# Kernel optimization log

Measured on AMD Instinct MI355X. Metric: run time of the kernel, lower is better.

## Reference

```python
import jax, jax.numpy as jnp
import numpy as np

B, C, P, E, M, H, K = 1024, 8192, 3, 64, 128, 16, 8
SCALE = 0.05
EPS = 1e-12  # tf.math.l2_normalize epsilon


def setup_inputs() -> dict:
    key = jax.random.key(0)
    ks = jax.random.split(key, 16)
    return {
        'pools': jax.random.uniform(ks[0], (B, C), dtype=jnp.float32),            # dense stand-in for SparseTensor batch_pools
        'metapaths': jax.random.uniform(ks[1], (P, C, C), dtype=jnp.float32),     # card-card metapath matrices
        'card_embeddings': jax.random.normal(ks[2], (C, E), dtype=jnp.float32) * SCALE,
        'mp_kernels': jax.random.normal(ks[3], (P, E, M), dtype=jnp.float32) * SCALE,
        'mp_biases': jnp.zeros((P, M, 1), dtype=jnp.float32),
        'Wq': jax.random.normal(ks[4], (M, H, K), dtype=jnp.float32) * SCALE,
        'bq': jnp.zeros((H, K), dtype=jnp.float32),
        'Wk': jax.random.normal(ks[5], (M, H, K), dtype=jnp.float32) * SCALE,
        'bk': jnp.zeros((H, K), dtype=jnp.float32),
        'Wv': jax.random.normal(ks[6], (M, H, K), dtype=jnp.float32) * SCALE,
        'bv': jnp.zeros((H, K), dtype=jnp.float32),
        'Wo': jax.random.normal(ks[7], (H, K, M), dtype=jnp.float32) * SCALE,
        'bo': jnp.zeros((M,), dtype=jnp.float32),
        'pool_kernel': jax.random.normal(ks[8], (M, E), dtype=jnp.float32) * SCALE,
        'pool_bias': jnp.zeros((E,), dtype=jnp.float32),
    }


def _l2_normalize(x, axis):
    # matches tf.math.l2_normalize: x / sqrt(max(sum(x^2), eps))
    sq = jnp.sum(jnp.square(x), axis=axis, keepdims=True)
    return x * jax.lax.rsqrt(jnp.maximum(sq, EPS))


def reference(pools, metapaths, card_embeddings, mp_kernels, mp_biases,
              Wq, bq, Wk, bk, Wv, bv, Wo, bo, pool_kernel, pool_bias):
    # --- MetapathEmbed layers, vectorized over the P metapaths ---
    # path_card_embeddings: act(einsum('ce,em->mc') + bias) -> (P, M, C)
    path_card = jax.nn.silu(jnp.einsum('ce,pem->pmc', card_embeddings, mp_kernels) + mp_biases)
    # path_card_matrix: einsum('mc,cd->dm') -> (P, C, M)
    pcm = jnp.einsum('pmc,pcd->pdm', path_card, metapaths)
    # sparse_dense_matmul(batch_pools, path_card_matrix); stack over metapaths -> (B, P, M)
    x = jnp.einsum('bd,pdm->bpm', pools, pcm)

    # --- keras MultiHeadAttention(query=x, value=x) ---
    q = jnp.einsum('bpm,mhk->bphk', x, Wq) + bq
    k = jnp.einsum('bpm,mhk->bphk', x, Wk) + bk
    v = jnp.einsum('bpm,mhk->bphk', x, Wv) + bv
    scores = jnp.einsum('bphk,bqhk->bhpq', q, k) / np.float32(np.sqrt(K))
    attn = jax.nn.softmax(scores, axis=-1)
    o = jnp.einsum('bhpq,bqhk->bphk', attn, v)
    attended = jnp.einsum('bphk,hkm->bpm', o, Wo) + bo  # (B, P, M)

    # --- pooling head ---
    pre_pool = jnp.sum(attended, axis=1)                       # (B, M)
    pool_embeds = jnp.einsum('bm,me->be', pre_pool, pool_kernel) + pool_bias
    norm_pool = _l2_normalize(pool_embeds, axis=1)             # (B, E)
    norm_cards = _l2_normalize(card_embeddings, axis=1)        # (C, E)
    return (jnp.einsum('be,ce->bc', norm_pool, norm_cards) + 1.0) / 2.0
```

## Files before the change

kernel.cpp:

```cpp
#include <hip/hip_runtime.h>
#include <hip/hip_bf16.h>

typedef unsigned int uint;
typedef unsigned short ushort;
typedef float f32x4 __attribute__((ext_vector_type(4)));
typedef short s16x8 __attribute__((ext_vector_type(8)));
typedef int i32x4 __attribute__((ext_vector_type(4)));
typedef uint u32x2 __attribute__((ext_vector_type(2)));

#define C_DIM 8192
#define B_DIM 1024
#define P_DIM 3
#define E_DIM 64
#define M_DIM 128

#define PCA_OFF   0ull
#define PART_OFF  15728640ull
#define PCMH_OFF  66060288ull
#define PCML_OFF  72351744ull
#define XPART_OFF PART_OFF
#define NPOOL_OFF 78643200ull
#define NCARD_OFF 78774272ull

__device__ __forceinline__ uint bf16_rne(float f) {
  uint u = __builtin_bit_cast(uint, f);
  return (u + 0x7fffu + ((u >> 16) & 1u)) >> 16;
}
__device__ __forceinline__ float bf16_to_f32(uint b) {
  return __builtin_bit_cast(float, b << 16);
}
__device__ __forceinline__ uint pk2(float a, float b) {
  float2 t; t.x = a; t.y = b;
  __hip_bfloat162 h2 = __float22bfloat162_rn(t);
  uint r;
  __builtin_memcpy(&r, &h2, 4);
  return r;
}

__global__ __launch_bounds__(256) void k1_pathcard(
    const float* __restrict__ cardemb, const float* __restrict__ mpk,
    const float* __restrict__ mpbias, ushort* __restrict__ pcA) {
  __shared__ float ce_l[64 * 68];
  const int tid = threadIdx.x;
  const int cb = blockIdx.x;
  const int p  = blockIdx.y;
  for (int r = 0; r < 16; ++r) {
    int i = r * 256 + tid;
    int row = i >> 6, col = i & 63;
    ce_l[row * 68 + col] = cardemb[(size_t)(cb * 64 + row) * 64 + col];
  }
  __syncthreads();
  const int m = tid & 127;
  const int chalf = tid >> 7;
  float kr[64];
#pragma unroll
  for (int e = 0; e < 64; ++e) kr[e] = mpk[(size_t)p * E_DIM * M_DIM + e * M_DIM + m];
  const float bias = mpbias[p * M_DIM + m];
  for (int cl0 = 0; cl0 < 32; ++cl0) {
    int cl = chalf * 32 + cl0;
    float acc = bias;
#pragma unroll
    for (int e = 0; e < 64; ++e) acc += ce_l[cl * 68 + e] * kr[e];
    float s = acc / (1.0f + expf(-acc));
    uint hb = bf16_rne(s);
    uint lb = bf16_rne(s - bf16_to_f32(hb));
    int c = cb * 64 + cl;
    int kt = c >> 5, kl = c & 31;
    size_t off = ((size_t)(p * 256 + kt) * 20480 + (size_t)m * 80 + (size_t)kl * 2) >> 1;
    pcA[off] = (ushort)hb;
    pcA[off + 5120] = (ushort)lb;
  }
}

__global__ __launch_bounds__(256, 3) void k2_big(
    const float* __restrict__ mp, const ushort* __restrict__ pcA,
    float* __restrict__ partial) {
  __shared__ char smem[32768];
  const int tid = threadIdx.x;
  int lin = blockIdx.x + 64 * (blockIdx.y + 4 * blockIdx.z);
  int swz = (lin & 7) * 96 + (lin >> 3);
  const int dt = swz & 63, q = (swz >> 6) & 3, p = swz >> 8;
  const int lane = tid & 63, wid = tid >> 6;
  const int wr = wid >> 1, wc = wid & 1;
  const int r16 = lane & 15, g4 = lane >> 4;
  const float* mpb = mp + (size_t)p * C_DIM * C_DIM + (size_t)dt * 128;
  const char* pcb = (const char*)pcA + (size_t)(p * 256 + q * 64) * 20480;
  const int sd = tid & 127, skh = tid >> 7;
  const int fc = ((sd ^ (sd >> 2)) & 3) << 4;
  const int fr = ((r16 ^ (r16 >> 2)) & 3) << 4;

  f32x4 acc[4][4];
#pragma unroll
  for (int i = 0; i < 4; ++i)
#pragma unroll
    for (int j = 0; j < 4; ++j) acc[i][j] = (f32x4){0.f, 0.f, 0.f, 0.f};

  float br[16];
  s16x8 ahA[4], alA[4], ahB[4], alB[4];

#define LOADA(T, AH, AL)                                                      \
  {                                                                           \
    const char* At_ = pcb + (size_t)(T) * 20480;                              \
    _Pragma("unroll") for (int i = 0; i < 4; ++i) {                           \
      int offa_ = (wr * 64 + i * 16 + r16) * 80 + g4 * 16;                    \
      AH[i] = *(const s16x8*)(At_ + offa_);                                   \
      AL[i] = *(const s16x8*)(At_ + 10240 + offa_);                           \
    }                                                                         \
  }
#define LOADB(T)                                                              \
  {                                                                           \
    int c0_ = q * 2048 + (T) * 32;                                            \
    _Pragma("unroll") for (int ii = 0; ii < 2; ++ii) {                        \
      const float* rp_ = mpb + (size_t)(c0_ + ii * 16 + skh * 8) * C_DIM + sd;\
      _Pragma("unroll") for (int j = 0; j < 8; ++j)                           \
          br[ii * 8 + j] = rp_[(size_t)j * C_DIM];                            \
    }                                                                         \
  }
#define WRITEB(BUF)                                                           \
  {                                                                           \
    char* bb_ = smem + (BUF) * 16384;                                         \
    _Pragma("unroll") for (int ii = 0; ii < 2; ++ii) {                        \
      uint hw_[4], lw_[4];                                                    \
      _Pragma("unroll") for (int k2 = 0; k2 < 4; ++k2) {                      \
        float v0_ = br[ii * 8 + k2 * 2], v1_ = br[ii * 8 + k2 * 2 + 1];       \
        uint h_ = pk2(v0_, v1_);                                              \
        float h0_ = __builtin_bit_cast(float, h_ << 16);                      \
        float h1_ = __builtin_bit_cast(float, h_ & 0xffff0000u);              \
        hw_[k2] = h_;                                                         \
        lw_[k2] = pk2(v0_ - h0_, v1_ - h1_);                                  \
      }                                                                       \
      int off_ = sd * 64 + ((((ii * 2 + skh) << 4)) ^ fc);                    \
      *(i32x4*)(bb_ + off_) =                                                 \
          (i32x4){(int)hw_[0], (int)hw_[1], (int)hw_[2], (int)hw_[3]};        \
      *(i32x4*)(bb_ + 8192 + off_) =                                          \
          (i32x4){(int)lw_[0], (int)lw_[1], (int)lw_[2], (int)lw_[3]};        \
    }                                                                         \
  }
#define MFMAB(BUF, AH, AL)                                                    \
  {                                                                           \
    const char* Bb_ = smem + (BUF) * 16384;                                   \
    _Pragma("unroll") for (int j = 0; j < 4; ++j) {                           \
      int offb_ = (wc * 64 + j * 16 + r16) * 64 + ((g4 << 4) ^ fr);           \
      s16x8 bh_ = *(const s16x8*)(Bb_ + offb_);                               \
      s16x8 bl_ = *(const s16x8*)(Bb_ + 8192 + offb_);                        \
      _Pragma("unroll") for (int i = 0; i < 4; ++i) {                         \
        acc[i][j] =                                                           \
            __builtin_amdgcn_mfma_f32_16x16x32_bf16(AH[i], bh_, acc[i][j], 0, 0, 0); \
        acc[i][j] =                                                           \
            __builtin_amdgcn_mfma_f32_16x16x32_bf16(AH[i], bl_, acc[i][j], 0, 0, 0); \
        acc[i][j] =                                                           \
            __builtin_amdgcn_mfma_f32_16x16x32_bf16(AL[i], bh_, acc[i][j], 0, 0, 0); \
      }                                                                       \
    }                                                                         \
  }

  LOADA(0, ahA, alA);
  asm volatile("" ::: "memory");
  LOADB(0);
  WRITEB(0);
  LOADB(1);
  asm volatile("s_waitcnt lgkmcnt(0)" ::: "memory");
  __builtin_amdgcn_s_barrier();
  __builtin_amdgcn_sched_barrier(0);

#define K2S(T, AHC, ALC, AHN, ALN)                                            \
  {                                                                           \
    MFMAB((T) & 1, AHC, ALC);                                                 \
    if ((T) < 63) {                                                           \
      WRITEB(((T) + 1) & 1);                                                  \
      LOADA((T) + 1, AHN, ALN);                                               \
      asm volatile("" ::: "memory");                                          \
      if ((T) + 2 < 64) LOADB((T) + 2);                                       \
      asm volatile("s_waitcnt lgkmcnt(0)" ::: "memory");                      \
      __builtin_amdgcn_s_barrier();                                           \
      __builtin_amdgcn_sched_barrier(0);                                      \
    }                                                                         \
  }

  for (int t2 = 0; t2 < 32; ++t2) {
    int t = 2 * t2;
    K2S(t, ahA, alA, ahB, alB);
    K2S(t + 1, ahB, alB, ahA, alA);
  }
#undef K2S
#undef MFMAB
#undef WRITEB
#undef LOADB
#undef LOADA

  float* part = partial + (size_t)(q * 3 + p) * M_DIM * C_DIM + (size_t)dt * 128;
#pragma unroll
  for (int i = 0; i < 4; ++i)
#pragma unroll
    for (int j = 0; j < 4; ++j)
#pragma unroll
      for (int r = 0; r < 4; ++r)
        part[(size_t)(wr * 64 + i * 16 + g4 * 4 + r) * C_DIM + (wc * 64 + j * 16 + r16)] =
            acc[i][j][r];
}

__global__ __launch_bounds__(256) void k2b_reduce(const float* __restrict__ p0,
                                                  ushort* __restrict__ oh,
                                                  ushort* __restrict__ ol) {
  size_t i = (size_t)blockIdx.x * 256 + threadIdx.x;
  f32x4 a = *(const f32x4*)(p0 + i * 4);
  f32x4 b = *(const f32x4*)(p0 + 3145728ull + i * 4);
  f32x4 c = *(const f32x4*)(p0 + 6291456ull + i * 4);
  f32x4 d = *(const f32x4*)(p0 + 9437184ull + i * 4);
  f32x4 s = (a + b) + (c + d);
  uint h[2], l[2];
#pragma unroll
  for (int k = 0; k < 2; ++k) {
    float v0 = s[k * 2], v1 = s[k * 2 + 1];
    uint hh = pk2(v0, v1);
    float h0 = __builtin_bit_cast(float, hh << 16);
    float h1 = __builtin_bit_cast(float, hh & 0xffff0000u);
    h[k] = hh;
    l[k] = pk2(v0 - h0, v1 - h1);
  }
  *(u32x2*)(oh + i * 4) = (u32x2){h[0], h[1]};
  *(u32x2*)(ol + i * 4) = (u32x2){l[0], l[1]};
}

__global__ __launch_bounds__(256, 4) void k3_x(const float* __restrict__ pools,
                                               const ushort* __restrict__ pcmh,
                                               const ushort* __restrict__ pcml,
                                               float* __restrict__ xpart) {
  const int tid = threadIdx.x;
  const int bt = blockIdx.x, ks = blockIdx.y;
  const int lane = tid & 63, w = tid >> 6;
  const int r16 = lane & 15, g4 = lane >> 4;
  const int rowbase = bt * 16;
  f32x4 acc[6];
#pragma unroll
  for (int j = 0; j < 6; ++j) acc[j] = (f32x4){0.f, 0.f, 0.f, 0.f};

  f32x4 pv0, pv1;
  {
    const float* ap = pools + (size_t)(rowbase + r16) * C_DIM + ks * 512 + g4 * 8;
    pv0 = *(const f32x4*)ap;
    pv1 = *(const f32x4*)(ap + 4);
  }

  for (int t = 0; t < 16; ++t) {
    int d0 = ks * 512 + t * 32 + g4 * 8;
    s16x8 ah, al;
    {
      i32x4 hw, lw;
#pragma unroll
      for (int k2 = 0; k2 < 4; ++k2) {
        float x0 = (k2 < 2) ? pv0[k2 * 2] : pv1[(k2 - 2) * 2];
        float x1 = (k2 < 2) ? pv0[k2 * 2 + 1] : pv1[(k2 - 2) * 2 + 1];
        uint h = pk2(x0, x1);
        float h0 = __builtin_bit_cast(float, h << 16);
        float h1 = __builtin_bit_cast(float, h & 0xffff0000u);
        hw[k2] = (int)h;
        lw[k2] = (int)pk2(x0 - h0, x1 - h1);
      }
      ah = __builtin_bit_cast(s16x8, hw);
      al = __builtin_bit_cast(s16x8, lw);
    }
    if (t < 15) {
      const float* ap = pools + (size_t)(rowbase + r16) * C_DIM + d0 + 32;
      pv0 = *(const f32x4*)ap;
      pv1 = *(const f32x4*)(ap + 4);
    }
#pragma unroll
    for (int j = 0; j < 6; ++j) {
      int col = w * 96 + j * 16 + r16;
      size_t boff = (size_t)col * C_DIM + d0;
      s16x8 bh = *(const s16x8*)(pcmh + boff);
      s16x8 bl = *(const s16x8*)(pcml + boff);
      acc[j] = __builtin_amdgcn_mfma_f32_16x16x32_bf16(ah, bh, acc[j], 0, 0, 0);
      acc[j] = __builtin_amdgcn_mfma_f32_16x16x32_bf16(ah, bl, acc[j], 0, 0, 0);
      acc[j] = __builtin_amdgcn_mfma_f32_16x16x32_bf16(al, bh, acc[j], 0, 0, 0);
    }
  }
#pragma unroll
  for (int j = 0; j < 6; ++j)
#pragma unroll
    for (int r = 0; r < 4; ++r) {
      int row = rowbase + g4 * 4 + r;
      int col = w * 96 + j * 16 + r16;
      int p = col >> 7, m = col & 127;
      xpart[((size_t)(ks * B_DIM + row) * 3 + p) * M_DIM + m] = acc[j][r];
    }
}

__global__ __launch_bounds__(128) void k4_attn(
    const float* __restrict__ xpart, const float* __restrict__ Wq,
    const float* __restrict__ bq, const float* __restrict__ Wk,
    const float* __restrict__ bk, const float* __restrict__ Wv,
    const float* __restrict__ bv, const float* __restrict__ Wo,
    const float* __restrict__ bo, const float* __restrict__ pk,
    const float* __restrict__ pb, ushort* __restrict__ npool) {
  __shared__ float xs[3 * 128], qa[3 * 128], ka[3 * 128], va[3 * 128], oa[3 * 128], pp[128];
  const int t = threadIdx.x;
  const int b = blockIdx.x;
#pragma unroll
  for (int p = 0; p < 3; ++p) {
    float v = 0.f;
    for (int ks = 0; ks < 16; ++ks)
      v += xpart[((size_t)(ks * B_DIM + b) * 3 + p) * M_DIM + t];
    xs[p * 128 + t] = v;
  }
  __syncthreads();
  float qv[3], kv[3], vv[3];
#pragma unroll
  for (int p = 0; p < 3; ++p) { qv[p] = bq[t]; kv[p] = bk[t]; vv[p] = bv[t]; }
  for (int m = 0; m < 128; ++m) {
    float wq = Wq[m * 128 + t], wk = Wk[m * 128 + t], wv = Wv[m * 128 + t];
#pragma unroll
    for (int p = 0; p < 3; ++p) {
      float xv = xs[p * 128 + m];
      qv[p] += xv * wq;
      kv[p] += xv * wk;
      vv[p] += xv * wv;
    }
  }
#pragma unroll
  for (int p = 0; p < 3; ++p) {
    qa[p * 128 + t] = qv[p];
    ka[p * 128 + t] = kv[p];
    va[p * 128 + t] = vv[p];
  }
  __syncthreads();
  const int h = t >> 3;
  float w[3][3];
#pragma unroll
  for (int p = 0; p < 3; ++p) {
    float s[3];
#pragma unroll
    for (int qq = 0; qq < 3; ++qq) {
      float d = 0.f;
#pragma unroll
      for (int kk = 0; kk < 8; ++kk)
        d += qa[p * 128 + h * 8 + kk] * ka[qq * 128 + h * 8 + kk];
      s[qq] = d / 2.8284271247461903f;
    }
    float mx = fmaxf(s[0], fmaxf(s[1], s[2]));
    float e0 = expf(s[0] - mx), e1 = expf(s[1] - mx), e2 = expf(s[2] - mx);
    float inv = 1.0f / (e0 + e1 + e2);
    w[p][0] = e0 * inv; w[p][1] = e1 * inv; w[p][2] = e2 * inv;
  }
#pragma unroll
  for (int p = 0; p < 3; ++p) {
    float o = w[p][0] * va[0 * 128 + t] + w[p][1] * va[1 * 128 + t] + w[p][2] * va[2 * 128 + t];
    oa[p * 128 + t] = o;
  }
  __syncthreads();
  float pre = 3.0f * bo[t];
#pragma unroll
  for (int p = 0; p < 3; ++p)
    for (int hk = 0; hk < 128; ++hk) pre += oa[p * 128 + hk] * Wo[hk * 128 + t];
  pp[t] = pre;
  __syncthreads();
  if (t < 64) {
    float pe = pb[t];
    for (int m = 0; m < 128; ++m) pe += pp[m] * pk[m * 64 + t];
    float ss = pe * pe;
#pragma unroll
    for (int off = 32; off; off >>= 1) ss += __shfl_xor(ss, off, 64);
    float rs = 1.0f / sqrtf(fmaxf(ss, 1e-12f));
    npool[b * 64 + t] = (ushort)bf16_rne(pe * rs);
  }
}

__global__ __launch_bounds__(256) void k4b_ncard(const float* __restrict__ ce,
                                                 ushort* __restrict__ ncard) {
  const int t = threadIdx.x;
  const int r = blockIdx.x * 4 + (t >> 6);
  const int lane = t & 63;
  float v = ce[(size_t)r * 64 + lane];
  float ss = v * v;
#pragma unroll
  for (int off = 32; off; off >>= 1) ss += __shfl_xor(ss, off, 64);
  float rs = 1.0f / sqrtf(fmaxf(ss, 1e-12f));
  ncard[(size_t)r * 64 + lane] = (ushort)bf16_rne(v * rs);
}

__global__ __launch_bounds__(256, 2) void k5_out(const ushort* __restrict__ np_,
                                                 const ushort* __restrict__ nc,
                                                 float* __restrict__ out) {
  const int tid = threadIdx.x;
  const int bt = blockIdx.x, ct = blockIdx.y;
  const int lane = tid & 63, wid = tid >> 6;
  const int wr = wid >> 1, wc = wid & 1;
  const int r16 = lane & 15, g4 = lane >> 4;
  f32x4 acc[4][4];
#pragma unroll
  for (int i = 0; i < 4; ++i)
#pragma unroll
    for (int j = 0; j < 4; ++j) acc[i][j] = (f32x4){0.f, 0.f, 0.f, 0.f};
#pragma unroll
  for (int ks = 0; ks < 2; ++ks) {
    int e0 = ks * 32 + g4 * 8;
    s16x8 af[4], bf_[4];
#pragma unroll
    for (int i = 0; i < 4; ++i)
      af[i] = *(const s16x8*)(np_ + (size_t)(bt * 128 + wr * 64 + i * 16 + r16) * 64 + e0);
#pragma unroll
    for (int j = 0; j < 4; ++j)
      bf_[j] = *(const s16x8*)(nc + (size_t)(ct * 128 + wc * 64 + j * 16 + r16) * 64 + e0);
#pragma unroll
    for (int i = 0; i < 4; ++i)
#pragma unroll
      for (int j = 0; j < 4; ++j)
        acc[i][j] = __builtin_amdgcn_mfma_f32_16x16x32_bf16(af[i], bf_[j], acc[i][j], 0, 0, 0);
  }
#pragma unroll
  for (int i = 0; i < 4; ++i)
#pragma unroll
    for (int j = 0; j < 4; ++j)
#pragma unroll
      for (int r = 0; r < 4; ++r) {
        int row = bt * 128 + wr * 64 + i * 16 + g4 * 4 + r;
        int col = ct * 128 + wc * 64 + j * 16 + r16;
        out[(size_t)row * C_DIM + col] = (acc[i][j][r] + 1.0f) * 0.5f;
      }
}

extern "C" void kernel_launch(void* const* d_in, const int* in_sizes, int n_in,
                              void* d_out, int out_size, void* d_ws, size_t ws_size,
                              hipStream_t stream) {
  const float* pools = (const float*)d_in[0];
  const float* metapaths = (const float*)d_in[1];
  const float* cardemb = (const float*)d_in[2];
  const float* mpk = (const float*)d_in[3];
  const float* mpbias = (const float*)d_in[4];
  const float* Wq = (const float*)d_in[5];
  const float* bq = (const float*)d_in[6];
  const float* Wk = (const float*)d_in[7];
  const float* bk = (const float*)d_in[8];
  const float* Wv = (const float*)d_in[9];
  const float* bv = (const float*)d_in[10];
  const float* Wo = (const float*)d_in[11];
  const float* bo = (const float*)d_in[12];
  const float* pk = (const float*)d_in[13];
  const float* pb = (const float*)d_in[14];
  float* out = (float*)d_out;
  char* ws = (char*)d_ws;

  ushort* pcA = (ushort*)(ws + PCA_OFF);
  float* part = (float*)(ws + PART_OFF);
  ushort* pcmh = (ushort*)(ws + PCMH_OFF);
  ushort* pcml = (ushort*)(ws + PCML_OFF);
  float* xpart = (float*)(ws + XPART_OFF);
  ushort* npool = (ushort*)(ws + NPOOL_OFF);
  ushort* ncard = (ushort*)(ws + NCARD_OFF);

  k1_pathcard<<<dim3(128, 3), dim3(256), 0, stream>>>(cardemb, mpk, mpbias, pcA);
  k2_big<<<dim3(64, 4, 3), dim3(256), 0, stream>>>(metapaths, pcA, part);
  k2b_reduce<<<dim3(3072), dim3(256), 0, stream>>>(part, pcmh, pcml);
  k3_x<<<dim3(64, 16), dim3(256), 0, stream>>>(pools, pcmh, pcml, xpart);
  k4b_ncard<<<dim3(2048), dim3(256), 0, stream>>>(cardemb, ncard);
  k4_attn<<<dim3(1024), dim3(128), 0, stream>>>(xpart, Wq, bq, Wk, bk, Wv, bv, Wo, bo, pk, pb,
                                                npool);
  k5_out<<<dim3(8, 64), dim3(256), 0, stream>>>(npool, ncard, out);
}
```

Before: 406.3 us.

## Deepen metapath-load prefetch in big GEMM and fold card normalization into k1

The main GEMM kernel now double-buffers the fp32 metapath register loads two tiles ahead and loads the A (path-card) fragments just in time rather than one step ahead. This trades A-fragment registers for a second B register buffer, aiming to hide more global-load latency on the dominant 3x8192x8192 stream. Separately, the card-embedding normalization is merged into k1 as an extra grid row, which removes one kernel launch. The register-allocation change risks pressure or spills and exposes A-load latency before the MFMAs.

```diff
diff --git a/kernel.cpp b/kernel.cpp
--- a/kernel.cpp
+++ b/kernel.cpp
@@ -39,11 +39,26 @@
 
 __global__ __launch_bounds__(256) void k1_pathcard(
     const float* __restrict__ cardemb, const float* __restrict__ mpk,
-    const float* __restrict__ mpbias, ushort* __restrict__ pcA) {
-  __shared__ float ce_l[64 * 68];
+    const float* __restrict__ mpbias, ushort* __restrict__ pcA,
+    ushort* __restrict__ ncard) {
   const int tid = threadIdx.x;
   const int cb = blockIdx.x;
   const int p  = blockIdx.y;
+  if (p == 3) {
+    const int lane = tid & 63;
+#pragma unroll
+    for (int g = 0; g < 16; ++g) {
+      int r = cb * 64 + g * 4 + (tid >> 6);
+      float v = cardemb[(size_t)r * 64 + lane];
+      float ss = v * v;
+#pragma unroll
+      for (int off = 32; off; off >>= 1) ss += __shfl_xor(ss, off, 64);
+      float rs = 1.0f / sqrtf(fmaxf(ss, 1e-12f));
+      ncard[(size_t)r * 64 + lane] = (ushort)bf16_rne(v * rs);
+    }
+    return;
+  }
+  __shared__ float ce_l[64 * 68];
   for (int r = 0; r < 16; ++r) {
     int i = r * 256 + tid;
     int row = i >> 6, col = i & 63;
@@ -95,34 +110,34 @@
 #pragma unroll
     for (int j = 0; j < 4; ++j) acc[i][j] = (f32x4){0.f, 0.f, 0.f, 0.f};
 
-  float br[16];
-  s16x8 ahA[4], alA[4], ahB[4], alB[4];
-
-#define LOADA(T, AH, AL)                                                      \
+  float brA[16], brB[16];
+  s16x8 ah[4], al[4];
+
+#define LOADA(T)                                                              \
   {                                                                           \
     const char* At_ = pcb + (size_t)(T) * 20480;                              \
     _Pragma("unroll") for (int i = 0; i < 4; ++i) {                           \
       int offa_ = (wr * 64 + i * 16 + r16) * 80 + g4 * 16;                    \
-      AH[i] = *(const s16x8*)(At_ + offa_);                                   \
-      AL[i] = *(const s16x8*)(At_ + 10240 + offa_);                           \
+      ah[i] = *(const s16x8*)(At_ + offa_);                                   \
+      al[i] = *(const s16x8*)(At_ + 10240 + offa_);                           \
     }                                                                         \
   }
-#define LOADB(T)                                                              \
+#define LOADB(T, BR)                                                          \
   {                                                                           \
     int c0_ = q * 2048 + (T) * 32;                                            \
     _Pragma("unroll") for (int ii = 0; ii < 2; ++ii) {                        \
       const float* rp_ = mpb + (size_t)(c0_ + ii * 16 + skh * 8) * C_DIM + sd;\
       _Pragma("unroll") for (int j = 0; j < 8; ++j)                           \
-          br[ii * 8 + j] = rp_[(size_t)j * C_DIM];                            \
+          BR[ii * 8 + j] = rp_[(size_t)j * C_DIM];                            \
     }                                                                         \
   }
-#define WRITEB(BUF)                                                           \
+#define WRITEB(BR, BUF)                                                       \
   {                                                                           \
     char* bb_ = smem + (BUF) * 16384;                                         \
     _Pragma("unroll") for (int ii = 0; ii < 2; ++ii) {                        \
       uint hw_[4], lw_[4];                                                    \
       _Pragma("unroll") for (int k2 = 0; k2 < 4; ++k2) {                      \
-        float v0_ = br[ii * 8 + k2 * 2], v1_ = br[ii * 8 + k2 * 2 + 1];       \
+        float v0_ = BR[ii * 8 + k2 * 2], v1_ = BR[ii * 8 + k2 * 2 + 1];       \
         uint h_ = pk2(v0_, v1_);                                              \
         float h0_ = __builtin_bit_cast(float, h_ << 16);                      \
         float h1_ = __builtin_bit_cast(float, h_ & 0xffff0000u);              \
@@ -136,7 +151,7 @@
           (i32x4){(int)lw_[0], (int)lw_[1], (int)lw_[2], (int)lw_[3]};        \
     }                                                                         \
   }
-#define MFMAB(BUF, AH, AL)                                                    \
+#define MFMAB(BUF)                                                            \
   {                                                                           \
     const char* Bb_ = smem + (BUF) * 16384;                                   \
     _Pragma("unroll") for (int j = 0; j < 4; ++j) {                           \
@@ -145,32 +160,30 @@
       s16x8 bl_ = *(const s16x8*)(Bb_ + 8192 + offb_);                        \
       _Pragma("unroll") for (int i = 0; i < 4; ++i) {                         \
         acc[i][j] =                                                           \
-            __builtin_amdgcn_mfma_f32_16x16x32_bf16(AH[i], bh_, acc[i][j], 0, 0, 0); \
+            __builtin_amdgcn_mfma_f32_16x16x32_bf16(ah[i], bh_, acc[i][j], 0, 0, 0); \
         acc[i][j] =                                                           \
-            __builtin_amdgcn_mfma_f32_16x16x32_bf16(AH[i], bl_, acc[i][j], 0, 0, 0); \
+            __builtin_amdgcn_mfma_f32_16x16x32_bf16(ah[i], bl_, acc[i][j], 0, 0, 0); \
         acc[i][j] =                                                           \
-            __builtin_amdgcn_mfma_f32_16x16x32_bf16(AL[i], bh_, acc[i][j], 0, 0, 0); \
+            __builtin_amdgcn_mfma_f32_16x16x32_bf16(al[i], bh_, acc[i][j], 0, 0, 0); \
       }                                                                       \
     }                                                                         \
   }
 
-  LOADA(0, ahA, alA);
-  asm volatile("" ::: "memory");
-  LOADB(0);
-  WRITEB(0);
-  LOADB(1);
+  LOADB(0, brA);
+  LOADB(1, brB);
+  WRITEB(brA, 0);
   asm volatile("s_waitcnt lgkmcnt(0)" ::: "memory");
   __builtin_amdgcn_s_barrier();
   __builtin_amdgcn_sched_barrier(0);
 
-#define K2S(T, AHC, ALC, AHN, ALN)                                            \
+#define K2S(T, BRL, BRW, TAIL)                                                \
   {                                                                           \
-    MFMAB((T) & 1, AHC, ALC);                                                 \
-    if ((T) < 63) {                                                           \
-      WRITEB(((T) + 1) & 1);                                                  \
-      LOADA((T) + 1, AHN, ALN);                                               \
-      asm volatile("" ::: "memory");                                          \
-      if ((T) + 2 < 64) LOADB((T) + 2);                                       \
+    LOADA(T);                                                                 \
+    asm volatile("" ::: "memory");                                            \
+    if ((T) < 62) LOADB((T) + 2, BRL);                                        \
+    MFMAB((T) & 1);                                                           \
+    if (!(TAIL)) {                                                            \
+      WRITEB(BRW, ((T) + 1) & 1);                                             \
       asm volatile("s_waitcnt lgkmcnt(0)" ::: "memory");                      \
       __builtin_amdgcn_s_barrier();                                           \
       __builtin_amdgcn_sched_barrier(0);                                      \
@@ -179,8 +192,8 @@
 
   for (int t2 = 0; t2 < 32; ++t2) {
     int t = 2 * t2;
-    K2S(t, ahA, alA, ahB, alB);
-    K2S(t + 1, ahB, alB, ahA, alA);
+    K2S(t, brA, brB, false);
+    K2S(t + 1, brB, brA, (t2 == 31));
   }
 #undef K2S
 #undef MFMAB
@@ -364,19 +377,6 @@
     float rs = 1.0f / sqrtf(fmaxf(ss, 1e-12f));
     npool[b * 64 + t] = (ushort)bf16_rne(pe * rs);
   }
-}
-
-__global__ __launch_bounds__(256) void k4b_ncard(const float* __restrict__ ce,
-                                                 ushort* __restrict__ ncard) {
-  const int t = threadIdx.x;
-  const int r = blockIdx.x * 4 + (t >> 6);
-  const int lane = t & 63;
-  float v = ce[(size_t)r * 64 + lane];
-  float ss = v * v;
-#pragma unroll
-  for (int off = 32; off; off >>= 1) ss += __shfl_xor(ss, off, 64);
-  float rs = 1.0f / sqrtf(fmaxf(ss, 1e-12f));
-  ncard[(size_t)r * 64 + lane] = (ushort)bf16_rne(v * rs);
 }
 
 __global__ __launch_bounds__(256, 2) void k5_out(const ushort* __restrict__ np_,
@@ -449,11 +449,10 @@
   ushort* npool = (ushort*)(ws + NPOOL_OFF);
   ushort* ncard = (ushort*)(ws + NCARD_OFF);
 
-  k1_pathcard<<<dim3(128, 3), dim3(256), 0, stream>>>(cardemb, mpk, mpbias, pcA);
+  k1_pathcard<<<dim3(128, 4), dim3(256), 0, stream>>>(cardemb, mpk, mpbias, pcA, ncard);
   k2_big<<<dim3(64, 4, 3), dim3(256), 0, stream>>>(metapaths, pcA, part);
   k2b_reduce<<<dim3(3072), dim3(256), 0, stream>>>(part, pcmh, pcml);
   k3_x<<<dim3(64, 16), dim3(256), 0, stream>>>(pools, pcmh, pcml, xpart);
-  k4b_ncard<<<dim3(2048), dim3(256), 0, stream>>>(cardemb, ncard);
   k4_attn<<<dim3(1024), dim3(128), 0, stream>>>(xpart, Wq, bq, Wk, bk, Wv, bv, Wo, bo, pk, pb,
                                                 npool);
   k5_out<<<dim3(8, 64), dim3(256), 0, stream>>>(npool, ncard, out);
```

New measurement: 389.9 us. -4.0%, faster.
